# Kernel tuning notes

Measured on AMD Instinct MI355X. Metric: run time of the kernel, lower is better.

## Reference

```python
import jax, jax.numpy as jnp
import numpy as np

# Mamba2 config (from AdapterMamba: d_model=1024, n_layer=4, headdim=32; mamba_ssm defaults)
D_MODEL = 1024
N_LAYER = 4
EXPAND = 2
HEADDIM = 32
D_STATE = 128
D_CONV = 4
NGROUPS = 1
D_INNER = EXPAND * D_MODEL            # 2048
NHEADS = D_INNER // HEADDIM           # 64
CONV_DIM = D_INNER + 2 * NGROUPS * D_STATE   # 2304
D_IN_PROJ = 2 * D_INNER + 2 * NGROUPS * D_STATE + NHEADS  # 4416
BATCH, SEQLEN = 4, 2048


def setup_inputs() -> dict:
    key = jax.random.key(0)
    ks = jax.random.split(key, 8)
    x = jax.random.normal(ks[0], (BATCH, SEQLEN, D_MODEL), jnp.float32)
    s_in = 1.0 / np.sqrt(D_MODEL)
    s_out = 1.0 / np.sqrt(D_INNER)
    W_in = jax.random.normal(ks[1], (N_LAYER, D_MODEL, D_IN_PROJ), jnp.float32) * s_in
    conv_w = jax.random.normal(ks[2], (N_LAYER, CONV_DIM, D_CONV), jnp.float32) * 0.5
    conv_b = jnp.zeros((N_LAYER, CONV_DIM), jnp.float32)
    # dt_bias = softplus^{-1}(dt) for dt in [1e-3, 0.1] (mamba dt_init)
    dt = jax.random.uniform(ks[3], (N_LAYER, NHEADS), jnp.float32, 0.001, 0.1)
    dt_bias = jnp.log(jnp.expm1(dt))
    # A in [1, 16] per head (A_init_range)
    A_log = jnp.log(jax.random.uniform(ks[4], (N_LAYER, NHEADS), jnp.float32, 1.0, 16.0))
    D = jnp.ones((N_LAYER, NHEADS), jnp.float32)
    gate_norm_w = jnp.ones((N_LAYER, D_INNER), jnp.float32)
    W_out = jax.random.normal(ks[5], (N_LAYER, D_INNER, D_MODEL), jnp.float32) * s_out
    block_norm_w = jnp.ones((N_LAYER, D_MODEL), jnp.float32)
    final_norm_w = jnp.ones((D_MODEL,), jnp.float32)
    return dict(x=x, W_in=W_in, conv_w=conv_w, conv_b=conv_b, dt_bias=dt_bias,
                A_log=A_log, D=D, gate_norm_w=gate_norm_w, W_out=W_out,
                block_norm_w=block_norm_w, final_norm_w=final_norm_w)


def _rmsnorm(x, w, eps=1e-5):
    return x * jax.lax.rsqrt(jnp.mean(x * x, axis=-1, keepdims=True) + eps) * w


def _mamba2_layer(h, Wi, cw, cb, dtb, Alog, Dh, gw, Wo):
    B, L, _ = h.shape
    zxbcdt = h @ Wi                                        # [B,L,4416]
    z, xBC, dt = jnp.split(zxbcdt, [D_INNER, D_INNER + CONV_DIM], axis=-1)
    # causal depthwise conv1d, width D_CONV, over (x, B, C) channels
    xp = jnp.pad(xBC, ((0, 0), (D_CONV - 1, 0), (0, 0)))
    conv = cb + sum(xp[:, k:k + L, :] * cw[:, k] for k in range(D_CONV))
    xBC = jax.nn.silu(conv)
    xs, Bm, Cm = jnp.split(xBC, [D_INNER, D_INNER + D_STATE], axis=-1)
    xs = xs.reshape(B, L, NHEADS, HEADDIM)                 # [B,L,H,P]
    dt = jax.nn.softplus(dt + dtb)                         # [B,L,H]
    A = -jnp.exp(Alog)                                     # [H]
    dA = jnp.exp(dt * A)                                   # [B,L,H]
    dtx = dt[..., None] * xs                               # [B,L,H,P]

    def step(hs, inp):
        dA_t, dtx_t, B_t, C_t = inp
        # hs: [B,H,P,N]
        hs = hs * dA_t[:, :, None, None] + dtx_t[..., None] * B_t[:, None, None, :]
        y = jnp.einsum('bhpn,bn->bhp', hs, C_t)
        return hs, y

    h0 = jnp.zeros((B, NHEADS, HEADDIM, D_STATE), h.dtype)
    _, ys = jax.lax.scan(step, h0, (dA.swapaxes(0, 1), dtx.swapaxes(0, 1),
                                    Bm.swapaxes(0, 1), Cm.swapaxes(0, 1)))
    y = ys.swapaxes(0, 1) + Dh[None, None, :, None] * xs   # skip term D*x
    y = y.reshape(B, L, D_INNER)
    y = _rmsnorm(y * jax.nn.silu(z), gw)                   # gated RMSNorm (Mamba2)
    return y @ Wo


def reference(x, W_in, conv_w, conv_b, dt_bias, A_log, D, gate_norm_w, W_out,
              block_norm_w, final_norm_w):
    h = x
    for l in range(N_LAYER):
        h = h + _mamba2_layer(_rmsnorm(h, block_norm_w[l]), W_in[l], conv_w[l],
                              conv_b[l], dt_bias[l], A_log[l], D[l],
                              gate_norm_w[l], W_out[l])
    return _rmsnorm(h, final_norm_w)
```

## Files before the change

### kernel.cpp

```cpp
#include <hip/hip_runtime.h>

typedef unsigned short u16;
typedef __bf16 bf16x8 __attribute__((ext_vector_type(8)));
typedef float f32x4 __attribute__((ext_vector_type(4)));
typedef u16 u16x8 __attribute__((ext_vector_type(8)));

#define NLAYER 4
#define DMODEL 1024
#define DINNER 2048
#define NHEADS 64
#define CONVDIM 2304
#define XBCLD 2368
#define DPROJ 4416
#define DPROJP 4608
#define BATCH 4
#define SEQLEN 2048
#define NTOK 8192
#define QC 64
#define NCH (SEQLEN / QC)

__device__ __forceinline__ u16 f2bf(float f) {
  union { float f; unsigned u; } v; v.f = f;
  return (u16)((v.u + 0x7fffu + ((v.u >> 16) & 1u)) >> 16);
}
__device__ __forceinline__ float bf2f(u16 h) {
  union { unsigned u; float f; } v; v.u = (unsigned)h << 16; return v.f;
}

__device__ __forceinline__ float block_sum256(float v) {
  __shared__ float red[4];
  #pragma unroll
  for (int o = 32; o; o >>= 1) v += __shfl_xor(v, o);
  int t = threadIdx.x;
  if ((t & 63) == 0) red[t >> 6] = v;
  __syncthreads();
  return red[0] + red[1] + red[2] + red[3];
}

__device__ __forceinline__ int swz128(int row, int g) { return (row << 7) + (((g ^ (row & 7)) << 3)); }
__device__ __forceinline__ int swz64(int row, int g)  { return (row << 6) + (((g ^ (row & 7)) << 3)); }

#define GLDS16(g, s) __builtin_amdgcn_global_load_lds( \
    (const __attribute__((address_space(1))) void*)(g), \
    (__attribute__((address_space(3))) void*)(s), 16, 0, 0)

template<int NF, int MODE>
__global__ __launch_bounds__(512, 1) void gemm256_k(
    const u16* __restrict__ A, const u16* __restrict__ Bt,
    float* __restrict__ C, u16* __restrict__ zy, u16* __restrict__ xbc,
    float* __restrict__ dtraw, int K, int nkt) {
  constexpr int NBH = (NF == 4) ? 2 : 1;
  __shared__ __align__(16) u16 As[2][2][128 * 64];
  __shared__ __align__(16) u16 Bs[2][NBH][128 * 64];

  const int tid = threadIdx.x;
  const int w = tid >> 6, l = tid & 63;
  const int wm = w >> 2, wn = w & 3;
  const int l16 = l & 15, kg = l >> 4;
  const int lr = l >> 3, lc = l & 7;
  const int swg = lc ^ lr;

  const int gx = gridDim.x;
  const int nwg = gx * gridDim.y;
  int bid = blockIdx.y * gx + blockIdx.x;
  bid = (bid & 7) * (nwg >> 3) + (bid >> 3);
  const int m0 = (bid / gx) << 8;
  const int n0 = (bid % gx) * (NF << 6);

  f32x4 acc[8][NF] = {};

  auto stage = [&](int buf, int kt) {
    const size_t kb = (size_t)(kt << 6) + (swg << 3);
    #pragma unroll
    for (int h = 0; h < 2; ++h)
      #pragma unroll
      for (int i = 0; i < 2; ++i)
        GLDS16(A + (size_t)(m0 + (h << 7) + (i << 6) + (w << 3) + lr) * K + kb,
               &As[buf][h][(i << 12) + (w << 9)]);
    #pragma unroll
    for (int h = 0; h < NBH; ++h)
      #pragma unroll
      for (int i = 0; i < 2; ++i)
        GLDS16(Bt + (size_t)(n0 + (h << 7) + (i << 6) + (w << 3) + lr) * K + kb,
               &Bs[buf][h][(i << 12) + (w << 9)]);
  };

  stage(0, 0);
  asm volatile("s_waitcnt vmcnt(0)" ::: "memory");
  __syncthreads();

  for (int kt = 0; kt < nkt; ++kt) {
    const int c = kt & 1;
    if (kt + 1 < nkt) stage(c ^ 1, kt + 1);

    bf16x8 breg[NF][2];
    #pragma unroll
    for (int nf = 0; nf < NF; ++nf)
      #pragma unroll
      for (int ks = 0; ks < 2; ++ks) {
        const int row = wn * (NF << 4) + (nf << 4) + l16;
        const int bh = row >> 7, r = row & 127;
        breg[nf][ks] = *(const bf16x8*)&Bs[c][bh][(r << 6) + ((((ks << 2) + kg) ^ (r & 7)) << 3)];
      }
    #pragma unroll
    for (int qm = 0; qm < 2; ++qm) {
      bf16x8 areg[4][2];
      #pragma unroll
      for (int mf = 0; mf < 4; ++mf)
        #pragma unroll
        for (int ks = 0; ks < 2; ++ks) {
          const int r = (qm << 6) + (mf << 4) + l16;
          areg[mf][ks] = *(const bf16x8*)&As[c][wm][(r << 6) + ((((ks << 2) + kg) ^ (r & 7)) << 3)];
        }
      __builtin_amdgcn_s_setprio(1);
      #pragma unroll
      for (int mf = 0; mf < 4; ++mf)
        #pragma unroll
        for (int nf = 0; nf < NF; ++nf)
          #pragma unroll
          for (int ks = 0; ks < 2; ++ks)
            acc[(qm << 2) + mf][nf] = __builtin_amdgcn_mfma_f32_16x16x32_bf16(
                areg[mf][ks], breg[nf][ks], acc[(qm << 2) + mf][nf], 0, 0, 0);
      __builtin_amdgcn_s_setprio(0);
    }
    asm volatile("s_waitcnt vmcnt(0)" ::: "memory");
    __syncthreads();
  }

  #pragma unroll
  for (int mf = 0; mf < 8; ++mf) {
    const int row = m0 + (wm << 7) + (mf << 4) + (kg << 2);
    #pragma unroll
    for (int nf = 0; nf < NF; ++nf) {
      const int col = n0 + wn * (NF << 4) + (nf << 4) + l16;
      #pragma unroll
      for (int r = 0; r < 4; ++r) {
        const float v = acc[mf][nf][r];
        const size_t rr = (size_t)(row + r);
        if (MODE == 0) {
          C[rr * DMODEL + col] += v;
        } else {
          if (col < DINNER)                zy[rr * DINNER + col] = f2bf(v);
          else if (col < DINNER + CONVDIM) xbc[rr * XBCLD + (col - DINNER)] = f2bf(v);
          else if (col < DPROJ)            dtraw[rr * 64 + (col - DINNER - CONVDIM)] = v;
        }
      }
    }
  }
}

__global__ __launch_bounds__(256) void transpose_cvt_k(
    const float* __restrict__ in, u16* __restrict__ out, int R, int Cin, int Cpad) {
  __shared__ float t[64][65];
  const int c0 = blockIdx.x << 6, r0 = blockIdx.y << 6;
  const int tx = threadIdx.x & 63, ty = threadIdx.x >> 6;
  #pragma unroll
  for (int i = 0; i < 16; ++i) {
    int r = ty + (i << 2);
    int cc = c0 + tx;
    t[r][tx] = (cc < Cin) ? in[(size_t)(r0 + r) * Cin + cc] : 0.f;
  }
  __syncthreads();
  #pragma unroll
  for (int i = 0; i < 16; ++i) {
    int c = ty + (i << 2);
    out[(size_t)(c0 + c) * R + r0 + tx] = f2bf(t[tx][c]);
  }
}

__global__ __launch_bounds__(256) void transpose_bf16_k(
    const u16* __restrict__ in, u16* __restrict__ out) {
  __shared__ __align__(16) u16 tl[64][72];
  const int c0 = blockIdx.x << 6, r0 = blockIdx.y << 6;
  const int tid = threadIdx.x;
  #pragma unroll
  for (int i = 0; i < 2; ++i) {
    int row = (tid >> 3) + (i << 5);
    int cs = tid & 7;
    *(int4*)&tl[row][cs << 3] =
        *(const int4*)&in[(size_t)(r0 + row) * CONVDIM + c0 + (cs << 3)];
  }
  __syncthreads();
  #pragma unroll
  for (int p = 0; p < 2; ++p) {
    int slot = tid + (p << 8);
    int c = slot >> 3, tb = slot & 7;
    u16x8 v;
    #pragma unroll
    for (int j = 0; j < 8; ++j) v[j] = tl[(tb << 3) + j][c];
    *(u16x8*)&out[(size_t)(c0 + c) * NTOK + r0 + (tb << 3)] = v;
  }
}

__global__ void copy_k(const float* __restrict__ in, float* __restrict__ out, int n4) {
  int i = blockIdx.x * blockDim.x + threadIdx.x;
  int stride = gridDim.x * blockDim.x;
  for (; i < n4; i += stride)
    *(f32x4*)&out[(size_t)i * 4] = *(const f32x4*)&in[(size_t)i * 4];
}

__global__ __launch_bounds__(256) void rmsnorm_bf16_k(
    const float* __restrict__ in, const float* __restrict__ w, u16* __restrict__ out) {
  const size_t row = blockIdx.x;
  const int t = threadIdx.x;
  f32x4 v = *(const f32x4*)&in[row * DMODEL + t * 4];
  float ss = block_sum256(v[0]*v[0] + v[1]*v[1] + v[2]*v[2] + v[3]*v[3]);
  float sc = rsqrtf(ss * (1.f / DMODEL) + 1e-5f);
  f32x4 wv = *(const f32x4*)&w[t * 4];
  ushort4 o;
  o.x = f2bf(v[0] * sc * wv[0]); o.y = f2bf(v[1] * sc * wv[1]);
  o.z = f2bf(v[2] * sc * wv[2]); o.w = f2bf(v[3] * sc * wv[3]);
  *(ushort4*)&out[row * DMODEL + t * 4] = o;
}

__global__ __launch_bounds__(256) void final_rmsnorm_k(
    const float* __restrict__ in, const float* __restrict__ w, float* __restrict__ out) {
  const size_t row = blockIdx.x;
  const int t = threadIdx.x;
  f32x4 v = *(const f32x4*)&in[row * DMODEL + t * 4];
  float ss = block_sum256(v[0]*v[0] + v[1]*v[1] + v[2]*v[2] + v[3]*v[3]);
  float sc = rsqrtf(ss * (1.f / DMODEL) + 1e-5f);
  f32x4 wv = *(const f32x4*)&w[t * 4];
  f32x4 o;
  #pragma unroll
  for (int j = 0; j < 4; ++j) o[j] = v[j] * sc * wv[j];
  *(f32x4*)&out[row * DMODEL + t * 4] = o;
}

__global__ __launch_bounds__(256) void conv_silu_k(
    const u16* __restrict__ xbc, const float* __restrict__ cw,
    const float* __restrict__ cb, u16* __restrict__ xact) {
  const int c = (blockIdx.x << 8) + threadIdx.x;
  const int b = blockIdx.y >> 8;
  const int t0 = (blockIdx.y & 255) << 3;
  const size_t rb = (size_t)b * SEQLEN + t0;
  const float w0 = cw[c*4], w1 = cw[c*4+1], w2 = cw[c*4+2], w3 = cw[c*4+3];
  const float bias = cb[c];
  const u16* src = xbc + c;
  float xm3 = t0 ? bf2f(src[(rb - 3) * XBCLD]) : 0.f;
  float xm2 = t0 ? bf2f(src[(rb - 2) * XBCLD]) : 0.f;
  float xm1 = t0 ? bf2f(src[(rb - 1) * XBCLD]) : 0.f;
  #pragma unroll
  for (int j = 0; j < 8; ++j) {
    float xc = bf2f(src[(rb + j) * XBCLD]);
    float a = bias + w0 * xm3 + w1 * xm2 + w2 * xm1 + w3 * xc;
    xact[(rb + j) * CONVDIM + c] = f2bf(a / (1.f + expf(-a)));
    xm3 = xm2; xm2 = xm1; xm1 = xc;
  }
}

__global__ __launch_bounds__(256, 2) void ssd_local_k(
    const u16* __restrict__ xact, const u16* __restrict__ XT,
    const u16* __restrict__ BT, const float* __restrict__ dtraw,
    const float* __restrict__ dt_bias, const float* __restrict__ A_log,
    const float* __restrict__ Dv, u16* __restrict__ ybuf,
    u16* __restrict__ Sg, float* __restrict__ etg, float* __restrict__ decayg) {
  __shared__ __align__(16) u16 Bs[64 * 128];
  __shared__ __align__(16) u16 U[128 * 64];
  __shared__ __align__(16) u16 Xt[32 * 64];
  __shared__ __align__(16) u16 Pl[64 * 64];
  __shared__ float cums[64], dts[64], fac[64];

  const int h = blockIdx.x, ch = blockIdx.y, b = blockIdx.z;
  const int tid = threadIdx.x, w = tid >> 6, l = tid & 63;
  const int l16 = l & 15, kg = l >> 4;
  const size_t tokb = (size_t)b * SEQLEN + (ch << 6);
  const size_t schunk = ((size_t)(b * 64 + h) << 5) + ch;

  const int srow = tid >> 2, sseg = tid & 3;
  int4 creg[4], breg[4], btreg[4];
  #pragma unroll
  for (int i = 0; i < 4; ++i) {
    creg[i] = *(const int4*)&xact[(tokb + srow) * CONVDIM + 2176 + (sseg << 5) + (i << 3)];
    breg[i] = *(const int4*)&xact[(tokb + srow) * CONVDIM + 2048 + (sseg << 5) + (i << 3)];
  }
  const int xrow = tid >> 3, xseg = tid & 7;
  int4 xreg = *(const int4*)&XT[(size_t)((h << 5) + xrow) * NTOK + tokb + (xseg << 3)];
  #pragma unroll
  for (int i = 0; i < 4; ++i)
    btreg[i] = *(const int4*)&BT[(size_t)(tid >> 1) * NTOK + tokb + ((((tid & 1) << 2) + i) << 3)];

  #pragma unroll
  for (int i = 0; i < 4; ++i) {
    *(int4*)&U[swz128(srow, (sseg << 2) + i)]  = creg[i];
    *(int4*)&Bs[swz128(srow, (sseg << 2) + i)] = breg[i];
  }
  *(int4*)&Xt[swz64(xrow, xseg)] = xreg;

  if (w == 0) {
    float raw = dtraw[(tokb + l) * 64 + h] + dt_bias[h];
    float dtv = raw > 20.f ? raw : log1pf(__expf(raw));
    float cv = -dtv * __expf(A_log[h]);
    #pragma unroll
    for (int d = 1; d < 64; d <<= 1) {
      float o = __shfl_up(cv, d);
      if (l >= d) cv += o;
    }
    float a63 = __shfl(cv, 63);
    cums[l] = cv; dts[l] = dtv; fac[l] = dtv * __expf(a63 - cv);
    etg[(schunk << 6) + l] = __expf(cv);
    if (l == 0) decayg[schunk] = __expf(a63);
  }
  const float Dh = Dv[h];
  __syncthreads();

  f32x4 gacc[4] = {};
  #pragma unroll
  for (int ks = 0; ks < 4; ++ks) {
    bf16x8 ac = *(const bf16x8*)&U[swz128((w << 4) + l16, (ks << 2) + kg)];
    #pragma unroll
    for (int j = 0; j < 4; ++j)
      if (j <= w) {
        bf16x8 bb = *(const bf16x8*)&Bs[swz128((j << 4) + l16, (ks << 2) + kg)];
        gacc[j] = __builtin_amdgcn_mfma_f32_16x16x32_bf16(ac, bb, gacc[j], 0, 0, 0);
      }
  }
  float c_t[4];
  #pragma unroll
  for (int r = 0; r < 4; ++r) c_t[r] = cums[(w << 4) + (kg << 2) + r];
  #pragma unroll
  for (int j = 0; j < 4; ++j) {
    const int s = (j << 4) + l16;
    const float c_s = cums[s], d_s = dts[s];
    #pragma unroll
    for (int r = 0; r < 4; ++r) {
      const int t = (w << 4) + (kg << 2) + r;
      float v = (s <= t) ? gacc[j][r] * __expf(c_t[r] - c_s) * d_s : 0.f;
      Pl[(t << 6) + ((((s >> 3) ^ (t & 7)) << 3) | (s & 7))] = f2bf(v);
    }
  }

  f32x4 y1[2] = {};
  const int nks = (w >> 1) + 1;
  for (int ks = 0; ks < nks; ++ks) {
    bf16x8 ap = *(const bf16x8*)&Pl[swz64((w << 4) + l16, (ks << 2) + kg)];
    #pragma unroll
    for (int pj = 0; pj < 2; ++pj) {
      bf16x8 bx = *(const bf16x8*)&Xt[swz64((pj << 4) + l16, (ks << 2) + kg)];
      y1[pj] = __builtin_amdgcn_mfma_f32_16x16x32_bf16(ap, bx, y1[pj], 0, 0, 0);
    }
  }
  #pragma unroll
  for (int r = 0; r < 4; ++r) {
    const int t = (w << 4) + (kg << 2) + r;
    #pragma unroll
    for (int pj = 0; pj < 2; ++pj) {
      const int p = (pj << 4) + l16;
      float xv = bf2f(Xt[(p << 6) + ((((t >> 3) ^ (p & 7)) << 3) | (t & 7))]);
      ybuf[(tokb + t) * DINNER + (h << 5) + p] = f2bf(y1[pj][r] + Dh * xv);
    }
  }

  __syncthreads();
  #pragma unroll
  for (int i = 0; i < 4; ++i)
    *(int4*)&U[swz64(tid >> 1, ((tid & 1) << 2) + i)] = btreg[i];
  __syncthreads();

  f32x4 sacc[2][2] = {};
  #pragma unroll
  for (int ks = 0; ks < 2; ++ks) {
    float f8[8];
    #pragma unroll
    for (int j = 0; j < 8; ++j) f8[j] = fac[(ks << 5) + (kg << 3) + j];
    #pragma unroll
    for (int pt = 0; pt < 2; ++pt) {
      bf16x8 xr = *(const bf16x8*)&Xt[swz64((pt << 4) + l16, (ks << 2) + kg)];
      bf16x8 xs;
      #pragma unroll
      for (int j = 0; j < 8; ++j) xs[j] = (__bf16)((float)xr[j] * f8[j]);
      #pragma unroll
      for (int nt = 0; nt < 2; ++nt) {
        bf16x8 bb = *(const bf16x8*)&U[swz64(((w << 1) + nt) * 16 + l16, (ks << 2) + kg)];
        sacc[pt][nt] = __builtin_amdgcn_mfma_f32_16x16x32_bf16(xs, bb, sacc[pt][nt], 0, 0, 0);
      }
    }
  }
  u16* sp = Sg + (schunk << 12);
  #pragma unroll
  for (int pt = 0; pt < 2; ++pt)
    #pragma unroll
    for (int nt = 0; nt < 2; ++nt)
      #pragma unroll
      for (int r = 0; r < 4; ++r) {
        const int pr = (pt << 4) + (kg << 2) + r;
        const int n = (w << 5) + (nt << 4) + l16;
        sp[(pr << 7) + n] = f2bf(sacc[pt][nt][r]);
      }
}

__global__ __launch_bounds__(256) void state_scan_k(
    u16* __restrict__ SH, const float* __restrict__ decayg) {
  const int bid = blockIdx.x;
  const size_t base = ((size_t)bid << 17) + ((size_t)threadIdx.x << 4);
  float acc[16] = {};
  u16x8 s0 = *(const u16x8*)&SH[base];
  u16x8 s1 = *(const u16x8*)&SH[base + 8];
  for (int ch = 0; ch < 32; ++ch) {
    const float d = decayg[(bid << 5) + ch];
    u16x8 n0 = {}, n1 = {};
    if (ch + 1 < 32) {
      n0 = *(const u16x8*)&SH[base + ((size_t)(ch + 1) << 12)];
      n1 = *(const u16x8*)&SH[base + ((size_t)(ch + 1) << 12) + 8];
    }
    u16x8 h0, h1;
    #pragma unroll
    for (int j = 0; j < 8; ++j) { h0[j] = f2bf(acc[j]); h1[j] = f2bf(acc[8 + j]); }
    *(u16x8*)&SH[base + ((size_t)ch << 12)] = h0;
    *(u16x8*)&SH[base + ((size_t)ch << 12) + 8] = h1;
    #pragma unroll
    for (int j = 0; j < 8; ++j) {
      acc[j]     = d * acc[j]     + bf2f(s0[j]);
      acc[8 + j] = d * acc[8 + j] + bf2f(s1[j]);
    }
    s0 = n0; s1 = n1;
  }
}

__global__ __launch_bounds__(256) void ssd_cross_k(
    const u16* __restrict__ xact, const u16* __restrict__ Hg,
    const float* __restrict__ etg, u16* __restrict__ ybuf) {
  __shared__ __align__(16) u16 Cs[64 * 128];
  __shared__ __align__(16) u16 Hb[32 * 128];
  __shared__ float etl[64];
  const int h = blockIdx.x, ch = blockIdx.y + 1, b = blockIdx.z;
  const int tid = threadIdx.x, w = tid >> 6, l = tid & 63;
  const int l16 = l & 15, kg = l >> 4;
  const size_t tokb = (size_t)b * SEQLEN + (ch << 6);
  const size_t schunk = ((size_t)(b * 64 + h) << 5) + ch;

  const int srow = tid >> 2, sseg = tid & 3;
  #pragma unroll
  for (int i = 0; i < 4; ++i) {
    int4 v = *(const int4*)&xact[(tokb + srow) * CONVDIM + 2176 + (sseg << 5) + (i << 3)];
    *(int4*)&Cs[swz128(srow, (sseg << 2) + i)] = v;
  }
  const int hp = tid >> 3, hseg = tid & 7;
  #pragma unroll
  for (int i = 0; i < 2; ++i) {
    int4 v = *(const int4*)&Hg[(schunk << 12) + (hp << 7) + (((hseg << 1) + i) << 3)];
    *(int4*)&Hb[swz128(hp, (hseg << 1) + i)] = v;
  }
  if (tid < 64) etl[tid] = etg[(schunk << 6) + tid];
  __syncthreads();

  f32x4 y2[2] = {};
  #pragma unroll
  for (int ks = 0; ks < 4; ++ks) {
    bf16x8 ac = *(const bf16x8*)&Cs[swz128((w << 4) + l16, (ks << 2) + kg)];
    #pragma unroll
    for (int pj = 0; pj < 2; ++pj) {
      bf16x8 bh = *(const bf16x8*)&Hb[swz128((pj << 4) + l16, (ks << 2) + kg)];
      y2[pj] = __builtin_amdgcn_mfma_f32_16x16x32_bf16(ac, bh, y2[pj], 0, 0, 0);
    }
  }
  #pragma unroll
  for (int r = 0; r < 4; ++r) {
    const int t = (w << 4) + (kg << 2) + r;
    const float et = etl[t];
    #pragma unroll
    for (int pj = 0; pj < 2; ++pj) {
      const int p = (pj << 4) + l16;
      const size_t a = (tokb + t) * DINNER + (h << 5) + p;
      ybuf[a] = f2bf(bf2f(ybuf[a]) + et * y2[pj][r]);
    }
  }
}

__global__ __launch_bounds__(256) void gate_rmsnorm_k(
    const u16* __restrict__ y, u16* __restrict__ zy, const float* __restrict__ gw) {
  const size_t row = blockIdx.x;
  const int t = threadIdx.x;
  bf16x8 yv = *(const bf16x8*)&y[row * DINNER + t * 8];
  bf16x8 zv = *(const bf16x8*)&zy[row * DINNER + t * 8];
  float val[8]; float ss = 0.f;
  #pragma unroll
  for (int j = 0; j < 8; ++j) {
    float z = (float)zv[j];
    float v = (float)yv[j] * (z / (1.f + expf(-z)));
    val[j] = v; ss += v * v;
  }
  ss = block_sum256(ss);
  float sc = rsqrtf(ss * (1.f / DINNER) + 1e-5f);
  ushort4 o0, o1;
  o0.x = f2bf(val[0]*sc*gw[t*8+0]); o0.y = f2bf(val[1]*sc*gw[t*8+1]);
  o0.z = f2bf(val[2]*sc*gw[t*8+2]); o0.w = f2bf(val[3]*sc*gw[t*8+3]);
  o1.x = f2bf(val[4]*sc*gw[t*8+4]); o1.y = f2bf(val[5]*sc*gw[t*8+5]);
  o1.z = f2bf(val[6]*sc*gw[t*8+6]); o1.w = f2bf(val[7]*sc*gw[t*8+7]);
  *(ushort4*)&zy[row * DINNER + t * 8] = o0;
  *(ushort4*)&zy[row * DINNER + t * 8 + 4] = o1;
}

extern "C" void kernel_launch(void* const* d_in, const int* in_sizes, int n_in,
                              void* d_out, int out_size, void* d_ws, size_t ws_size,
                              hipStream_t stream) {
  const float* x       = (const float*)d_in[0];
  const float* W_in    = (const float*)d_in[1];
  const float* conv_w  = (const float*)d_in[2];
  const float* conv_b  = (const float*)d_in[3];
  const float* dt_bias = (const float*)d_in[4];
  const float* A_log   = (const float*)d_in[5];
  const float* Dv      = (const float*)d_in[6];
  const float* gate_w  = (const float*)d_in[7];
  const float* W_out   = (const float*)d_in[8];
  const float* block_w = (const float*)d_in[9];
  const float* final_w = (const float*)d_in[10];
  float* out = (float*)d_out;

  char* p = (char*)d_ws;
  auto alloc = [&](size_t bytes) { char* r = p; p += (bytes + 255) & ~(size_t)255; return r; };
  float* hbuf  = (float*)alloc((size_t)NTOK * DMODEL * 4);
  u16*   slabA = (u16*)  alloc((size_t)NTOK * DINNER * 2);
  u16*   slabB = (u16*)  alloc((size_t)NTOK * DINNER * 2);
  u16*   slabC = (u16*)  alloc((size_t)NTOK * CONVDIM * 2);
  u16*   xbcXT = (u16*)  alloc((size_t)NTOK * XBCLD * 2);
  float* dtraw = (float*)alloc((size_t)NTOK * NHEADS * 4);
  u16*   BT    = (u16*)  alloc((size_t)128 * NTOK * 2);
  if ((size_t)(p - (char*)d_ws) > ws_size) return;

  u16*   Sg     = (u16*)  alloc((size_t)BATCH * NHEADS * NCH * 4096 * 2);
  float* etg    = (float*)alloc((size_t)BATCH * NHEADS * NCH * 64 * 4);
  float* decayg = (float*)alloc((size_t)BATCH * NHEADS * NCH * 4);
  const bool par = ((size_t)(p - (char*)d_ws) <= ws_size);

  u16* hn   = slabA;
  u16* ybuf = slabA;
  u16* wt   = slabC;
  u16* xact = slabC;
  u16* xbc  = xbcXT;
  u16* XT   = xbcXT;

  copy_k<<<2048, 256, 0, stream>>>(x, hbuf, NTOK * DMODEL / 4);

  for (int l = 0; l < NLAYER; ++l) {
    rmsnorm_bf16_k<<<NTOK, 256, 0, stream>>>(hbuf, block_w + l * DMODEL, hn);
    transpose_cvt_k<<<dim3(DPROJP/64, DMODEL/64), 256, 0, stream>>>(
        W_in + (size_t)l * DMODEL * DPROJ, wt, DMODEL, DPROJ, DPROJP);
    gemm256_k<4, 1><<<dim3(DPROJP/256, NTOK/256), 512, 0, stream>>>(
        hn, wt, nullptr, slabB, xbc, dtraw, DMODEL, DMODEL / 64);
    conv_silu_k<<<dim3(CONVDIM/256, BATCH * SEQLEN / 8), 256, 0, stream>>>(
        xbc, conv_w + (size_t)l * CONVDIM * 4, conv_b + (size_t)l * CONVDIM, xact);
    transpose_bf16_k<<<dim3(DINNER/64, NTOK/64), 256, 0, stream>>>(xact, XT);
    transpose_bf16_k<<<dim3(2, NTOK/64), 256, 0, stream>>>(xact + DINNER, BT);
    if (par) {
      ssd_local_k<<<dim3(NHEADS, NCH, BATCH), 256, 0, stream>>>(
          xact, XT, BT, dtraw, dt_bias + l * NHEADS, A_log + l * NHEADS,
          Dv + l * NHEADS, ybuf, Sg, etg, decayg);
      state_scan_k<<<BATCH * NHEADS, 256, 0, stream>>>(Sg, decayg);
      ssd_cross_k<<<dim3(NHEADS, NCH - 1, BATCH), 256, 0, stream>>>(
          xact, Sg, etg, ybuf);
    }
    gate_rmsnorm_k<<<NTOK, 256, 0, stream>>>(ybuf, slabB, gate_w + (size_t)l * DINNER);
    transpose_cvt_k<<<dim3(DMODEL/64, DINNER/64), 256, 0, stream>>>(
        W_out + (size_t)l * DINNER * DMODEL, wt, DINNER, DMODEL, DMODEL);
    gemm256_k<2, 0><<<dim3(DMODEL/128, NTOK/256), 512, 0, stream>>>(
        slabB, wt, hbuf, nullptr, nullptr, nullptr, DINNER, DINNER / 64);
  }
  final_rmsnorm_k<<<NTOK, 256, 0, stream>>>(hbuf, final_w, out);
}
```

Before: 1.612 ms.

## Restructure GEMM main loop into eight-phase ping-pong with interleaved staged loads

Replaces the two-buffer GEMM loop with an eight-phase schedule per pair of K tiles. A and B tile loads are split into half-tiles and issued between MFMA phases, with explicit barriers, sched_barriers and partial vmcnt waits. The aim is to overlap global-to-LDS traffic with MFMA work and to shorten the whole-tile synchronisation stalls. The cost is more barriers per K tile, more complex buffer reuse hazards, and a loop that assumes an even number of K tiles.

```diff
diff --git a/kernel.cpp b/kernel.cpp
--- a/kernel.cpp
+++ b/kernel.cpp
@@ -44,12 +44,36 @@
     (const __attribute__((address_space(1))) void*)(g), \
     (__attribute__((address_space(3))) void*)(s), 16, 0, 0)
 
+#define PH_READ(buf, p)                                                        \
+  if ((p) == 0) {                                                              \
+    _Pragma("unroll") for (int nf = 0; nf < NF; ++nf)                          \
+    _Pragma("unroll") for (int ks = 0; ks < 2; ++ks)                           \
+      breg[nf][ks] = readB(buf, nf, ks);                                       \
+  }                                                                            \
+  _Pragma("unroll") for (int i = 0; i < 2; ++i)                                \
+  _Pragma("unroll") for (int ks = 0; ks < 2; ++ks)                             \
+    ar[i][ks] = readA(buf, ((p) << 1) + i, ks);
+
+#define PH_TAIL(buf, p)                                                        \
+  __builtin_amdgcn_sched_barrier(0);                                           \
+  __builtin_amdgcn_s_barrier();                                                \
+  asm volatile("s_waitcnt lgkmcnt(0)" ::: "memory");                           \
+  __builtin_amdgcn_sched_barrier(0);                                           \
+  __builtin_amdgcn_s_setprio(1);                                               \
+  _Pragma("unroll") for (int i = 0; i < 2; ++i)                                \
+  _Pragma("unroll") for (int nf = 0; nf < NF; ++nf)                            \
+  _Pragma("unroll") for (int ks = 0; ks < 2; ++ks)                             \
+    acc[((p) << 1) + i][nf] = __builtin_amdgcn_mfma_f32_16x16x32_bf16(         \
+        ar[i][ks], breg[nf][ks], acc[((p) << 1) + i][nf], 0, 0, 0);            \
+  __builtin_amdgcn_s_setprio(0);                                               \
+  __builtin_amdgcn_s_barrier();
+
 template<int NF, int MODE>
-__global__ __launch_bounds__(512, 1) void gemm256_k(
+__global__ __launch_bounds__(512, 1) void gemm8p_k(
     const u16* __restrict__ A, const u16* __restrict__ Bt,
     float* __restrict__ C, u16* __restrict__ zy, u16* __restrict__ xbc,
-    float* __restrict__ dtraw, int K, int nkt) {
-  constexpr int NBH = (NF == 4) ? 2 : 1;
+    float* __restrict__ dtraw, int K, int nt2) {
+  constexpr int NBH = NF / 2;
   __shared__ __align__(16) u16 As[2][2][128 * 64];
   __shared__ __align__(16) u16 Bs[2][NBH][128 * 64];
 
@@ -68,63 +92,71 @@
   const int n0 = (bid % gx) * (NF << 6);
 
   f32x4 acc[8][NF] = {};
-
-  auto stage = [&](int buf, int kt) {
+  bf16x8 breg[NF][2];
+  bf16x8 ar[2][2];
+
+  auto stageA = [&](int buf, int h, int kt) {
     const size_t kb = (size_t)(kt << 6) + (swg << 3);
     #pragma unroll
-    for (int h = 0; h < 2; ++h)
-      #pragma unroll
-      for (int i = 0; i < 2; ++i)
-        GLDS16(A + (size_t)(m0 + (h << 7) + (i << 6) + (w << 3) + lr) * K + kb,
-               &As[buf][h][(i << 12) + (w << 9)]);
-    #pragma unroll
-    for (int h = 0; h < NBH; ++h)
-      #pragma unroll
-      for (int i = 0; i < 2; ++i)
-        GLDS16(Bt + (size_t)(n0 + (h << 7) + (i << 6) + (w << 3) + lr) * K + kb,
-               &Bs[buf][h][(i << 12) + (w << 9)]);
+    for (int j = 0; j < 2; ++j)
+      GLDS16(A + (size_t)(m0 + (h << 7) + (j << 6) + (w << 3) + lr) * K + kb,
+             &As[buf][h][(j << 12) + (w << 9)]);
   };
-
-  stage(0, 0);
+  auto stageB = [&](int buf, int h, int kt) {
+    const size_t kb = (size_t)(kt << 6) + (swg << 3);
+    #pragma unroll
+    for (int j = 0; j < 2; ++j)
+      GLDS16(Bt + (size_t)(n0 + (h << 7) + (j << 6) + (w << 3) + lr) * K + kb,
+             &Bs[buf][h][(j << 12) + (w << 9)]);
+  };
+  auto readA = [&](int buf, int mf, int ks) -> bf16x8 {
+    const int r = (mf << 4) + l16;
+    return *(const bf16x8*)&As[buf][wm][(r << 6) + ((((ks << 2) + kg) ^ (r & 7)) << 3)];
+  };
+  auto readB = [&](int buf, int nf, int ks) -> bf16x8 {
+    const int row = wn * (NF << 4) + (nf << 4) + l16;
+    const int bh = row >> 7, r = row & 127;
+    return *(const bf16x8*)&Bs[buf][bh][(r << 6) + ((((ks << 2) + kg) ^ (r & 7)) << 3)];
+  };
+
+  stageA(0, 0, 0); stageA(0, 1, 0);
+  #pragma unroll
+  for (int h = 0; h < NBH; ++h) stageB(0, h, 0);
+  #pragma unroll
+  for (int h = 0; h < NBH; ++h) stageB(1, h, 1);
   asm volatile("s_waitcnt vmcnt(0)" ::: "memory");
   __syncthreads();
 
-  for (int kt = 0; kt < nkt; ++kt) {
-    const int c = kt & 1;
-    if (kt + 1 < nkt) stage(c ^ 1, kt + 1);
-
-    bf16x8 breg[NF][2];
-    #pragma unroll
-    for (int nf = 0; nf < NF; ++nf)
-      #pragma unroll
-      for (int ks = 0; ks < 2; ++ks) {
-        const int row = wn * (NF << 4) + (nf << 4) + l16;
-        const int bh = row >> 7, r = row & 127;
-        breg[nf][ks] = *(const bf16x8*)&Bs[c][bh][(r << 6) + ((((ks << 2) + kg) ^ (r & 7)) << 3)];
-      }
-    #pragma unroll
-    for (int qm = 0; qm < 2; ++qm) {
-      bf16x8 areg[4][2];
-      #pragma unroll
-      for (int mf = 0; mf < 4; ++mf)
-        #pragma unroll
-        for (int ks = 0; ks < 2; ++ks) {
-          const int r = (qm << 6) + (mf << 4) + l16;
-          areg[mf][ks] = *(const bf16x8*)&As[c][wm][(r << 6) + ((((ks << 2) + kg) ^ (r & 7)) << 3)];
-        }
-      __builtin_amdgcn_s_setprio(1);
-      #pragma unroll
-      for (int mf = 0; mf < 4; ++mf)
-        #pragma unroll
-        for (int nf = 0; nf < NF; ++nf)
-          #pragma unroll
-          for (int ks = 0; ks < 2; ++ks)
-            acc[(qm << 2) + mf][nf] = __builtin_amdgcn_mfma_f32_16x16x32_bf16(
-                areg[mf][ks], breg[nf][ks], acc[(qm << 2) + mf][nf], 0, 0, 0);
-      __builtin_amdgcn_s_setprio(0);
-    }
-    asm volatile("s_waitcnt vmcnt(0)" ::: "memory");
-    __syncthreads();
+  for (int t = 0; t < nt2; ++t) {
+    const int kt0 = t << 1;
+    const bool more = (t + 1 < nt2);
+    PH_READ(0, 0)
+    stageA(1, 0, kt0 + 1);
+    PH_TAIL(0, 0)
+    PH_READ(0, 1)
+    stageA(1, 1, kt0 + 1);
+    PH_TAIL(0, 1)
+    PH_READ(0, 2)
+    if (more) stageB(0, 0, kt0 + 2);
+    PH_TAIL(0, 2)
+    PH_READ(0, 3)
+    if (more && NBH == 2) stageB(0, 1, kt0 + 2);
+    if (more) { asm volatile("s_waitcnt vmcnt(%0)" :: "n"(2 * NBH) : "memory"); }
+    else      { asm volatile("s_waitcnt vmcnt(0)" ::: "memory"); }
+    PH_TAIL(0, 3)
+    PH_READ(1, 0)
+    if (more) stageA(0, 0, kt0 + 2);
+    PH_TAIL(1, 0)
+    PH_READ(1, 1)
+    if (more) stageA(0, 1, kt0 + 2);
+    PH_TAIL(1, 1)
+    PH_READ(1, 2)
+    if (more) stageB(1, 0, kt0 + 3);
+    PH_TAIL(1, 2)
+    PH_READ(1, 3)
+    if (more && NBH == 2) stageB(1, 1, kt0 + 3);
+    if (more) { asm volatile("s_waitcnt vmcnt(%0)" :: "n"(2 * NBH) : "memory"); }
+    PH_TAIL(1, 3)
   }
 
   #pragma unroll
@@ -536,8 +568,8 @@
     rmsnorm_bf16_k<<<NTOK, 256, 0, stream>>>(hbuf, block_w + l * DMODEL, hn);
     transpose_cvt_k<<<dim3(DPROJP/64, DMODEL/64), 256, 0, stream>>>(
         W_in + (size_t)l * DMODEL * DPROJ, wt, DMODEL, DPROJ, DPROJP);
-    gemm256_k<4, 1><<<dim3(DPROJP/256, NTOK/256), 512, 0, stream>>>(
-        hn, wt, nullptr, slabB, xbc, dtraw, DMODEL, DMODEL / 64);
+    gemm8p_k<4, 1><<<dim3(DPROJP/256, NTOK/256), 512, 0, stream>>>(
+        hn, wt, nullptr, slabB, xbc, dtraw, DMODEL, DMODEL / 128);
     conv_silu_k<<<dim3(CONVDIM/256, BATCH * SEQLEN / 8), 256, 0, stream>>>(
         xbc, conv_w + (size_t)l * CONVDIM * 4, conv_b + (size_t)l * CONVDIM, xact);
     transpose_bf16_k<<<dim3(DINNER/64, NTOK/64), 256, 0, stream>>>(xact, XT);
@@ -553,8 +585,8 @@
     gate_rmsnorm_k<<<NTOK, 256, 0, stream>>>(ybuf, slabB, gate_w + (size_t)l * DINNER);
     transpose_cvt_k<<<dim3(DMODEL/64, DINNER/64), 256, 0, stream>>>(
         W_out + (size_t)l * DINNER * DMODEL, wt, DINNER, DMODEL, DMODEL);
-    gemm256_k<2, 0><<<dim3(DMODEL/128, NTOK/256), 512, 0, stream>>>(
-        slabB, wt, hbuf, nullptr, nullptr, nullptr, DINNER, DINNER / 64);
+    gemm8p_k<2, 0><<<dim3(DMODEL/128, NTOK/256), 512, 0, stream>>>(
+        slabB, wt, hbuf, nullptr, nullptr, nullptr, DINNER, DINNER / 128);
   }
   final_rmsnorm_k<<<NTOK, 256, 0, stream>>>(hbuf, final_w, out);
 }
```

After: 1.578 ms. -2.2%, faster.
